# Kernel optimization log

Measured on AMD Instinct MI355X. Metric: run time of the kernel, lower is better.

## Reference

```python
import jax, jax.numpy as jnp
import numpy as np

N, E, DIM, NF, ED = 15000, 30000, 64, 3, 1

def _gru_cell(x, h, w_ih, w_hh, b_ih, b_hh):
    gi = x @ w_ih.T + b_ih
    gh = h @ w_hh.T + b_hh
    ir, iz, i_n = jnp.split(gi, 3, axis=-1)
    hr, hz, hn = jnp.split(gh, 3, axis=-1)
    r = jax.nn.sigmoid(ir + hr)
    z = jax.nn.sigmoid(iz + hz)
    n = jnp.tanh(i_n + r * hn)
    return (1.0 - z) * n + z * h

def _lstm_cell(x, h, c, w_ih, w_hh, b_ih, b_hh):
    g = x @ w_ih.T + b_ih + h @ w_hh.T + b_hh
    i, f, gg, o = jnp.split(g, 4, axis=-1)
    c2 = jax.nn.sigmoid(f) * c + jax.nn.sigmoid(i) * jnp.tanh(gg)
    return jax.nn.sigmoid(o) * jnp.tanh(c2), c2

def setup_inputs():
    key = jax.random.key(0)
    ks = jax.random.split(key, 32)
    p = lambda k, shape: jax.random.normal(k, shape, jnp.float32) * 0.05
    return {
        "x": jax.random.normal(ks[0], (N, NF), jnp.float32),
        "edge_index": jax.random.randint(ks[1], (2, E), 0, N),
        "edge_attr": jax.random.uniform(ks[2], (E, ED), jnp.float32),
        "lin0_w": p(ks[3], (DIM, NF)), "lin0_b": p(ks[4], (DIM,)),
        "e1_w": p(ks[5], (DIM, ED)), "e1_b": p(ks[6], (DIM,)),
        "e2_w": p(ks[7], (DIM * DIM, DIM)), "e2_b": p(ks[8], (DIM * DIM,)),
        "root_w": p(ks[9], (DIM, DIM)), "conv_b": p(ks[10], (DIM,)),
        "gru_w_ih": p(ks[11], (3 * DIM, DIM)), "gru_w_hh": p(ks[12], (3 * DIM, DIM)),
        "gru_b_ih": p(ks[13], (3 * DIM,)), "gru_b_hh": p(ks[14], (3 * DIM,)),
        "s2s_w_ih": p(ks[15], (4 * DIM, 2 * DIM)), "s2s_w_hh": p(ks[16], (4 * DIM, DIM)),
        "s2s_b_ih": p(ks[17], (4 * DIM,)), "s2s_b_hh": p(ks[18], (4 * DIM,)),
        "mem_w_ih": p(ks[19], (4 * DIM, 2 * DIM)), "mem_w_hh": p(ks[20], (4 * DIM, DIM)),
        "mem_b_ih": p(ks[21], (4 * DIM,)), "mem_b_hh": p(ks[22], (4 * DIM,)),
        "lin1_w": p(ks[23], (DIM, DIM)), "lin1_b": p(ks[24], (DIM,)),
        "lin3_w": p(ks[25], (1, DIM)), "lin3_b": p(ks[26], (1,)),
    }

def reference(x, edge_index, edge_attr, lin0_w, lin0_b, e1_w, e1_b, e2_w, e2_b,
              root_w, conv_b, gru_w_ih, gru_w_hh, gru_b_ih, gru_b_hh,
              s2s_w_ih, s2s_w_hh, s2s_b_ih, s2s_b_hh,
              mem_w_ih, mem_w_hh, mem_b_ih, mem_b_hh,
              lin1_w, lin1_b, lin3_w, lin3_b):
    n = x.shape[0]
    src, dst = edge_index[0], edge_index[1]
    # per-edge weight matrices from the edge MLP: [E, DIM, DIM] (edge_attr is constant across the 6 conv steps)
    he = jax.nn.relu(edge_attr @ e1_w.T + e1_b)
    We = (he @ e2_w.T + e2_b).reshape(-1, DIM, DIM)
    deg = jax.ops.segment_sum(jnp.ones(src.shape[0], jnp.float32), dst, num_segments=n)
    denom = jnp.maximum(deg, 1.0)[:, None]
    out = jax.nn.relu(x @ lin0_w.T + lin0_b)   # [N, DIM]
    h = out                                    # GRU hidden init = lin0 output
    for _ in range(6):
        msg = jnp.einsum('ei,eio->eo', out[src], We)          # gather + per-edge matmul
        agg = jax.ops.segment_sum(msg, dst, num_segments=n) / denom  # mean aggr
        m = jax.nn.relu(agg + out @ root_w + conv_b)          # NNConv root + bias
        h = _gru_cell(m, h, gru_w_ih, gru_w_hh, gru_b_ih, gru_b_hh)
        out = h
    # Set2Set pooling over a single graph (data.batch is all zeros)
    q_star = jnp.zeros((1, 2 * DIM), x.dtype)
    hs = jnp.zeros((1, DIM), x.dtype)
    cs = jnp.zeros((1, DIM), x.dtype)
    for _ in range(6):
        hs, cs = _lstm_cell(q_star, hs, cs, s2s_w_ih, s2s_w_hh, s2s_b_ih, s2s_b_hh)
        e = out @ hs[0]                     # [N] attention logits
        a = jax.nn.softmax(e)
        r = (a[:, None] * out).sum(0, keepdims=True)  # [1, DIM]
        q_star = jnp.concatenate([hs, r], axis=-1)     # [1, 2*DIM]
    hx, cx = _lstm_cell(q_star, jnp.zeros((1, DIM), x.dtype), jnp.zeros((1, DIM), x.dtype),
                        mem_w_ih, mem_w_hh, mem_b_ih, mem_b_hh)
    o = jax.nn.relu(hx @ lin1_w.T + lin1_b)
    v = o @ lin3_w.T + lin3_b               # [1, 1]
    return v, hx, cx
```

## Files before the change

### kernel.cpp

```cpp
#include <hip/hip_runtime.h>
#include <math.h>

#define Nn 15000
#define NP 15040
#define Ee 30000
#define NB_E 118
#define EB 938

#define OFF_AGG   0
#define OFF_DEG   962560
#define ZERO_END  977560
#define OFF_OUT   977568
#define OFF_DINV  1940128
#define OFF_AT    1955136
#define OFF_BT    2221376
#define OFF_PE    2496016
#define OFF_BH    2526016
#define OFF_SS    2541376
#define OFF_SD    2571376
#define OFF_SA    2601376
#define OFF_SP    2631376
#define OFF_PK    2661376
#define OFF_GMA   2690048
#define OFF_GSA   2690304
#define OFF_GRA   2690560
#define OFF_GMB   2706944
#define OFF_GSB   2707200
#define OFF_GRB   2707456
#define OFF_TSA   2723968
#define OFF_TSB   2740352
#define OFF_TMA   2756736
#define OFF_TMB   2773120
#define OFF_HSA   2789504
#define OFF_CSA   2789568
#define OFF_HSB   2789632
#define OFF_CSB   2789696
#define WS_FLOATS 2789760

#define SA_L0_END   3760
#define SA_WT2_END  3872
#define SA_WT3_END  4128
#define SA_Z_END    5083
#define SA_AB_END   6123
#define SA_EP_END   6241
#define ZERO_F4     244390

__device__ __forceinline__ float sigf(float x) { return 1.0f / (1.0f + expf(-x)); }
__device__ __forceinline__ float bcast(float v, int l) {
    return __int_as_float(__builtin_amdgcn_readlane(__float_as_int(v), l));
}
__device__ __forceinline__ int bcasti(int v, int l) {
    return __builtin_amdgcn_readlane(v, l);
}

__global__ __launch_bounds__(256) void k_setupAll(
        const float* __restrict__ x, const float* __restrict__ l0w,
        const float* __restrict__ l0b, float* __restrict__ out,
        const float* __restrict__ e1w, const float* __restrict__ e1b,
        const float* __restrict__ e2w, const float* __restrict__ e2b,
        float* __restrict__ At, float* __restrict__ Bt,
        const float* __restrict__ rootw, const float* __restrict__ whh,
        const float* __restrict__ wih, float* __restrict__ pk,
        const float* __restrict__ swih, const float* __restrict__ swhh,
        const float* __restrict__ mwih,
        float* __restrict__ tsa, float* __restrict__ tsb,
        float* __restrict__ tma, float* __restrict__ tmb,
        float* __restrict__ zbase,
        const int* __restrict__ ei, const float* __restrict__ ea,
        float* __restrict__ deg, int* __restrict__ pe, int* __restrict__ bh) {
    int b = blockIdx.x, tid = threadIdx.x;
    if (b < SA_L0_END) {
        int idx = b*256 + tid;
        int n = idx >> 6, o = idx & 63;
        float vv = 0.f;
        if (n < Nn)
            vv = fmaxf(l0b[o] + x[n*3+0]*l0w[o*3+0] + x[n*3+1]*l0w[o*3+1]
                       + x[n*3+2]*l0w[o*3+2], 0.f);
        out[idx] = vv;
    } else if (b < SA_WT2_END) {
        int idx = (b - SA_L0_END)*256 + tid;
        int g = idx >> 12;
        int t2 = idx & 4095;
        int q4 = t2 >> 2, k = t2 & 3;
        int lane = q4 & 63;
        int i4 = q4 >> 6;
        int i = i4*4 + k;
        float vv;
        if (g == 0)      vv = rootw[i*64 + lane];
        else if (g < 4)  vv = whh[((g-1)*64 + lane)*64 + i];
        else             vv = wih[((g-4)*64 + lane)*64 + i];
        pk[idx] = vv;
    } else if (b < SA_WT3_END) {
        int idx = (b - SA_WT2_END)*256 + tid;
        int t2 = idx >> 14, r = idx & 16383;
        int i = r >> 8, g = r & 255;
        if (t2 == 0)      tsa[r] = swih[g*128 + i] + swhh[g*64 + i];
        else if (t2 == 1) tsb[r] = swih[g*128 + 64 + i];
        else if (t2 == 2) tma[r] = mwih[g*128 + i];
        else              tmb[r] = mwih[g*128 + 64 + i];
    } else if (b < SA_Z_END) {
        int idx = (b - SA_WT3_END)*256 + tid;
        if (idx < ZERO_F4)
            ((float4*)zbase)[idx] = make_float4(0.f, 0.f, 0.f, 0.f);
    } else if (b < SA_AB_END) {
        __shared__ float t[64]; __shared__ int valid[64];
        __shared__ float sbp[65]; __shared__ int cnt;
        __shared__ float su[64], sv[64];
        int rel = b - SA_Z_END;
        int j = rel >> 4, qc = rel & 15;
        float w1 = 0.f, b1 = 0.f, tv = 0.f; int va = 0;
        if (tid < 64) {
            w1 = e1w[tid]; b1 = e1b[tid];
            if (w1 != 0.f) { tv = -b1 / w1; va = (tv > 0.f && tv < 1.f) ? 1 : 0; }
            t[tid] = tv; valid[tid] = va;
        }
        __syncthreads();
        if (tid < 64 && va) {
            int rank = 0;
            for (int kk = 0; kk < 64; ++kk)
                if (valid[kk] && (t[kk] < tv || (t[kk] == tv && kk < tid))) rank++;
            sbp[rank] = tv;
        }
        if (tid == 0) { int c = 0; for (int kk = 0; kk < 64; ++kk) c += valid[kk]; cnt = c; }
        __syncthreads();
        int m = cnt;
        if (j > m) return;
        if (tid < 64) {
            float lo = (j == 0) ? 0.f : sbp[j-1];
            float hi = (j == m) ? 1.f : sbp[j];
            float c = 0.5f * (lo + hi);
            int msk = (c * w1 + b1) > 0.f;
            su[tid] = msk ? w1 : 0.f;
            sv[tid] = msk ? b1 : 0.f;
        }
        __syncthreads();
        int q = qc*256 + tid;
        int i = q >> 6, o = q & 63;
        const float* row = e2w + q*64;
        float a = 0.f, bb = 0.f;
        #pragma unroll 8
        for (int k = 0; k < 64; ++k) { float w = row[k]; a = fmaf(su[k], w, a); bb = fmaf(sv[k], w, bb); }
        At[j*4096 + o*64 + i] = a;
        Bt[j*4096 + o*64 + i] = bb + e2b[q];
    } else {
        __shared__ float t[64]; __shared__ int valid[64];
        __shared__ float sbp[65]; __shared__ int cnt;
        __shared__ int lh[65];
        int eb = b - SA_AB_END;
        float w1 = 0.f, b1 = 0.f, tv = 0.f; int va = 0;
        if (tid < 64) {
            w1 = e1w[tid]; b1 = e1b[tid];
            if (w1 != 0.f) { tv = -b1 / w1; va = (tv > 0.f && tv < 1.f) ? 1 : 0; }
            t[tid] = tv; valid[tid] = va;
        }
        if (tid < 65) lh[tid] = 0;
        __syncthreads();
        if (tid < 64 && va) {
            int rank = 0;
            for (int kk = 0; kk < 64; ++kk)
                if (valid[kk] && (t[kk] < tv || (t[kk] == tv && kk < tid))) rank++;
            sbp[rank] = tv;
        }
        if (tid == 0) { int c = 0; for (int kk = 0; kk < 64; ++kk) c += valid[kk]; cnt = c; }
        __syncthreads();
        int m = cnt;
        int e = eb * 256 + tid;
        if (e < Ee) {
            atomicAdd(&deg[ei[Ee + e]], 1.0f);
            float a = ea[e];
            int p = 0;
            for (int jj = 0; jj < m; ++jj) p += (sbp[jj] <= a) ? 1 : 0;
            pe[e] = p;
            atomicAdd(&lh[p], 1);
        }
        __syncthreads();
        if (tid < 65) bh[eb*65 + tid] = lh[tid];
    }
}

__global__ __launch_bounds__(256) void k_scatter3(
        const float* __restrict__ deg, float* __restrict__ dinv,
        const int* __restrict__ ei, const float* __restrict__ ea,
        const int* __restrict__ pe, const int* __restrict__ bh,
        int* __restrict__ sS, int* __restrict__ sD,
        float* __restrict__ sA, int* __restrict__ sP) {
    int tid = threadIdx.x;
    if (blockIdx.x < 59) {
        int n = blockIdx.x * 256 + tid;
        if (n < Nn) dinv[n] = 1.0f / fmaxf(deg[n], 1.0f);
        return;
    }
    int eb = blockIdx.x - 59;
    __shared__ int stot[65], sown[65], sbase[65], cur[65];
    if (tid < 65) {
        int own = 0, tot = 0;
        for (int b2 = 0; b2 < NB_E; ++b2) {
            int v = bh[b2*65 + tid];
            if (b2 < eb) own += v;
            tot += v;
        }
        stot[tid] = tot; sown[tid] = own;
    }
    __syncthreads();
    if (tid == 0) {
        int run = 0;
        for (int j = 0; j < 65; ++j) { sbase[j] = run; run += stot[j]; }
    }
    __syncthreads();
    if (tid < 65) cur[tid] = sbase[tid] + sown[tid];
    __syncthreads();
    int e = eb * 256 + tid;
    if (e >= Ee) return;
    int p = pe[e];
    int pos = atomicAdd(&cur[p], 1);
    sS[pos] = ei[e]; sD[pos] = ei[Ee + e]; sA[pos] = ea[e]; sP[pos] = p;
}

__global__ __launch_bounds__(256) void k_edge6(
        const int* __restrict__ sS, const int* __restrict__ sD,
        const float* __restrict__ sA, const int* __restrict__ sP,
        const float* __restrict__ out, const float* __restrict__ At,
        const float* __restrict__ Bt, const float* __restrict__ dinv,
        float* __restrict__ agg) {
    int tid = threadIdx.x, lane = tid & 63;
    int wid = (blockIdx.x * 256 + tid) >> 6;
    int e0 = wid * 8;
    if (e0 >= Ee) return;

    int eidx = e0 + lane;
    int msrc = 0, mdst = 0, mp = 0; float ma = 0.f, mdv = 0.f;
    if (lane < 8) {
        msrc = sS[eidx]; mdst = sD[eidx]; ma = sA[eidx]; mp = sP[eidx];
        mdv = dinv[mdst];
    }

    float hv[8];
    #pragma unroll
    for (int j = 0; j < 8; ++j) hv[j] = out[bcasti(msrc, j)*64 + lane];

    float Ar[64], Br[64];
    int curp = -1;
    #pragma unroll
    for (int j = 0; j < 8; ++j) {
        int p = bcasti(mp, j);
        if (p != curp) {
            curp = p;
            const float4* Ap4 = (const float4*)(At + p*4096 + lane*64);
            const float4* Bp4 = (const float4*)(Bt + p*4096 + lane*64);
            #pragma unroll
            for (int q = 0; q < 16; ++q) {
                float4 av = Ap4[q], bv = Bp4[q];
                Ar[q*4+0]=av.x; Ar[q*4+1]=av.y; Ar[q*4+2]=av.z; Ar[q*4+3]=av.w;
                Br[q*4+0]=bv.x; Br[q*4+1]=bv.y; Br[q*4+2]=bv.z; Br[q*4+3]=bv.w;
            }
        }
        float a = bcast(ma, j);
        float acc0 = 0.f, acc1 = 0.f, acc2 = 0.f, acc3 = 0.f;
        #pragma unroll
        for (int i = 0; i < 64; i += 4) {
            acc0 = fmaf(bcast(hv[j], i+0), fmaf(a, Ar[i+0], Br[i+0]), acc0);
            acc1 = fmaf(bcast(hv[j], i+1), fmaf(a, Ar[i+1], Br[i+1]), acc1);
            acc2 = fmaf(bcast(hv[j], i+2), fmaf(a, Ar[i+2], Br[i+2]), acc2);
            acc3 = fmaf(bcast(hv[j], i+3), fmaf(a, Ar[i+3], Br[i+3]), acc3);
        }
        float acc = ((acc0 + acc1) + (acc2 + acc3)) * bcast(mdv, j);
        atomicAdd(&agg[bcasti(mdst, j)*64 + lane], acc);
    }
}

__global__ __launch_bounds__(512, 2) void k_gru9(
        float* __restrict__ out, float* __restrict__ agg,
        const float* __restrict__ pk, const float* __restrict__ convb,
        const float* __restrict__ gbih, const float* __restrict__ gbhh) {
    __shared__ __align__(16) float wL[7*4096];
    int tid = threadIdx.x, lane = tid & 63, w = tid >> 6;
    int n0 = blockIdx.x*64 + w*8;

    float hv[8], av[8];
    #pragma unroll
    for (int k = 0; k < 8; ++k) hv[k] = out[(n0+k)*64 + lane];
    #pragma unroll
    for (int k = 0; k < 8; ++k) {
        int gi = (n0+k)*64 + lane;
        av[k] = agg[gi];
        agg[gi] = 0.f;
    }

    {
        const float4* src = (const float4*)pk;
        float4* dst = (float4*)wL;
        #pragma unroll
        for (int i = 0; i < 14; ++i) dst[i*512 + tid] = src[i*512 + tid];
    }
    __syncthreads();
    const float4* wL4 = (const float4*)wL;

    float mv[8], ghr[8], ghz[8], ghn[8];
    float a0[8], a1[8], a2[8], a3[8];
    #pragma unroll
    for (int k = 0; k < 8; ++k) { a0[k]=0.f; a1[k]=0.f; a2[k]=0.f; a3[k]=0.f; }
    #pragma unroll 4
    for (int i4 = 0; i4 < 16; ++i4) {
        float4 w0 = wL4[(0*16+i4)*64 + lane];
        float4 w1 = wL4[(1*16+i4)*64 + lane];
        float4 w2 = wL4[(2*16+i4)*64 + lane];
        float4 w3 = wL4[(3*16+i4)*64 + lane];
        #pragma unroll
        for (int k = 0; k < 8; ++k) {
            float h;
            h = bcast(hv[k], i4*4+0);
            a0[k]=fmaf(h,w0.x,a0[k]); a1[k]=fmaf(h,w1.x,a1[k]);
            a2[k]=fmaf(h,w2.x,a2[k]); a3[k]=fmaf(h,w3.x,a3[k]);
            h = bcast(hv[k], i4*4+1);
            a0[k]=fmaf(h,w0.y,a0[k]); a1[k]=fmaf(h,w1.y,a1[k]);
            a2[k]=fmaf(h,w2.y,a2[k]); a3[k]=fmaf(h,w3.y,a3[k]);
            h = bcast(hv[k], i4*4+2);
            a0[k]=fmaf(h,w0.z,a0[k]); a1[k]=fmaf(h,w1.z,a1[k]);
            a2[k]=fmaf(h,w2.z,a2[k]); a3[k]=fmaf(h,w3.z,a3[k]);
            h = bcast(hv[k], i4*4+3);
            a0[k]=fmaf(h,w0.w,a0[k]); a1[k]=fmaf(h,w1.w,a1[k]);
            a2[k]=fmaf(h,w2.w,a2[k]); a3[k]=fmaf(h,w3.w,a3[k]);
        }
    }
    float cbv = convb[lane];
    #pragma unroll
    for (int k = 0; k < 8; ++k) {
        mv[k] = fmaxf(a0[k] + av[k] + cbv, 0.f);
        ghr[k] = a1[k]; ghz[k] = a2[k]; ghn[k] = a3[k];
    }

    #pragma unroll
    for (int k = 0; k < 8; ++k) { a0[k]=0.f; a1[k]=0.f; a2[k]=0.f; }
    #pragma unroll 4
    for (int i4 = 0; i4 < 16; ++i4) {
        float4 w4v = wL4[(4*16+i4)*64 + lane];
        float4 w5v = wL4[(5*16+i4)*64 + lane];
        float4 w6v = wL4[(6*16+i4)*64 + lane];
        #pragma unroll
        for (int k = 0; k < 8; ++k) {
            float h;
            h = bcast(mv[k], i4*4+0);
            a0[k]=fmaf(h,w4v.x,a0[k]); a1[k]=fmaf(h,w5v.x,a1[k]); a2[k]=fmaf(h,w6v.x,a2[k]);
            h = bcast(mv[k], i4*4+1);
            a0[k]=fmaf(h,w4v.y,a0[k]); a1[k]=fmaf(h,w5v.y,a1[k]); a2[k]=fmaf(h,w6v.y,a2[k]);
            h = bcast(mv[k], i4*4+2);
            a0[k]=fmaf(h,w4v.z,a0[k]); a1[k]=fmaf(h,w5v.z,a1[k]); a2[k]=fmaf(h,w6v.z,a2[k]);
            h = bcast(mv[k], i4*4+3);
            a0[k]=fmaf(h,w4v.w,a0[k]); a1[k]=fmaf(h,w5v.w,a1[k]); a2[k]=fmaf(h,w6v.w,a2[k]);
        }
    }

    float br  = gbih[lane]      + gbhh[lane];
    float bz  = gbih[64+lane]   + gbhh[64+lane];
    float bnI = gbih[128+lane];
    float bnH = gbhh[128+lane];
    #pragma unroll
    for (int k = 0; k < 8; ++k) {
        float r  = sigf(a0[k] + ghr[k] + br);
        float z  = sigf(a1[k] + ghz[k] + bz);
        float nn = tanhf(fmaf(r, ghn[k] + bnH, a2[k] + bnI));
        out[(n0+k)*64 + lane] = (1.f - z)*nn + z*hv[k];
    }
}

__global__ __launch_bounds__(512) void k_s2s(
        const float* __restrict__ tsa, const float* __restrict__ tsb,
        const float* __restrict__ bih, const float* __restrict__ bhh,
        const float* __restrict__ hs_rd, const float* __restrict__ cs_rd,
        float* __restrict__ hs_wr, float* __restrict__ cs_wr,
        const float* __restrict__ out,
        const float* __restrict__ gmax_rd, const float* __restrict__ gsum_rd,
        const float* __restrict__ gr_rd,
        float* __restrict__ gmax_wr, float* __restrict__ gsum_wr,
        float* __restrict__ gr_wr, int it) {
    __shared__ float red[512], shs[64], scs[64], srv[64], sg[256];
    __shared__ float wred[8], zred[8];
    __shared__ float sm_m[8], sm_z[8], sm_r[8][64];
    int tid = threadIdx.x, lane = tid & 63, w = tid >> 6;
    if (it == 0) {
        if (tid < 64) { shs[tid] = 0.f; scs[tid] = 0.f; srv[tid] = 0.f; }
        __syncthreads();
    } else {
        float gm = (tid < 256) ? gmax_rd[tid] : -3.4e38f;
        float wm = gm;
        #pragma unroll
        for (int off = 32; off > 0; off >>= 1) wm = fmaxf(wm, __shfl_xor(wm, off, 64));
        if (lane == 0) wred[w] = wm;
        __syncthreads();
        float M = fmaxf(fmaxf(fmaxf(wred[0], wred[1]), fmaxf(wred[2], wred[3])),
                        fmaxf(fmaxf(wred[4], wred[5]), fmaxf(wred[6], wred[7])));
        float zt = (tid < 256) ? gsum_rd[tid] * expf(gm - M) : 0.f;
        #pragma unroll
        for (int off = 32; off > 0; off >>= 1) zt += __shfl_xor(zt, off, 64);
        if (lane == 0) zred[w] = zt;
        float racc = 0.f;
        for (int b2 = w; b2 < 256; b2 += 8)
            racc = fmaf(gr_rd[b2*64 + lane], expf(gmax_rd[b2] - M), racc);
        red[tid] = racc;
        if (tid < 64) { shs[tid] = hs_rd[tid]; scs[tid] = cs_rd[tid]; }
        __syncthreads();
        if (w == 0) {
            float Z = zred[0]+zred[1]+zred[2]+zred[3]+zred[4]+zred[5]+zred[6]+zred[7];
            float s = 0.f;
            #pragma unroll
            for (int k = 0; k < 8; ++k) s += red[k*64 + lane];
            srv[lane] = s / Z;
        }
        __syncthreads();
    }
    if (tid < 256) {
        float g = bih[tid] + bhh[tid];
        #pragma unroll 8
        for (int i = 0; i < 64; ++i)
            g += shs[i]*tsa[i*256 + tid] + srv[i]*tsb[i*256 + tid];
        sg[tid] = g;
    }
    __syncthreads();
    if (tid < 64) {
        float ii = sigf(sg[tid]), ff = sigf(sg[64+tid]);
        float gg = tanhf(sg[128+tid]), oo = sigf(sg[192+tid]);
        float c2 = ff*scs[tid] + ii*gg;
        float hn = oo*tanhf(c2);
        shs[tid] = hn;
        if (blockIdx.x == 0) { hs_wr[tid] = hn; cs_wr[tid] = c2; }
    }
    __syncthreads();
    float hsv = shs[lane];
    float m = -3.4e38f, Z2 = 0.f, racc2 = 0.f;
    for (int n = blockIdx.x*8 + w; n < Nn; n += 2048) {
        float ov = out[n*64 + lane];
        float p = ov * hsv;
        #pragma unroll
        for (int off = 32; off > 0; off >>= 1) p += __shfl_xor(p, off, 64);
        float mn = fmaxf(m, p);
        float sc = expf(m - mn);
        float t  = expf(p - mn);
        Z2 = fmaf(Z2, sc, t);
        racc2 = fmaf(racc2, sc, t*ov);
        m = mn;
    }
    if (lane == 0) { sm_m[w] = m; sm_z[w] = Z2; }
    sm_r[w][lane] = racc2;
    __syncthreads();
    if (w == 0) {
        float M = sm_m[0];
        #pragma unroll
        for (int j = 1; j < 8; ++j) M = fmaxf(M, sm_m[j]);
        float Zb = 0.f, rb = 0.f;
        #pragma unroll
        for (int j = 0; j < 8; ++j) {
            float e = expf(sm_m[j] - M);
            Zb = fmaf(sm_z[j], e, Zb);
            rb = fmaf(sm_r[j][lane], e, rb);
        }
        gr_wr[blockIdx.x*64 + lane] = rb;
        if (lane == 0) { gmax_wr[blockIdx.x] = M; gsum_wr[blockIdx.x] = Zb; }
    }
}

__global__ __launch_bounds__(256) void k_final2(
        const float* __restrict__ tma, const float* __restrict__ tmb,
        const float* __restrict__ mbih, const float* __restrict__ mbhh,
        const float* __restrict__ hs,
        const float* __restrict__ gmax, const float* __restrict__ gsum,
        const float* __restrict__ gr,
        const float* __restrict__ l1w, const float* __restrict__ l1b,
        const float* __restrict__ l3w, const float* __restrict__ l3b,
        float* __restrict__ dout) {
    __shared__ float red[256], shs[64], srv[64], sg[256], shx[64], so[64];
    __shared__ float wred[4], zred[4];
    int tid = threadIdx.x, lane = tid & 63, w = tid >> 6;
    {
        float gm = gmax[tid];
        float wm = gm;
        #pragma unroll
        for (int off = 32; off > 0; off >>= 1) wm = fmaxf(wm, __shfl_xor(wm, off, 64));
        if (lane == 0) wred[w] = wm;
        __syncthreads();
        float M = fmaxf(fmaxf(wred[0], wred[1]), fmaxf(wred[2], wred[3]));
        float zt = gsum[tid] * expf(gm - M);
        #pragma unroll
        for (int off = 32; off > 0; off >>= 1) zt += __shfl_xor(zt, off, 64);
        if (lane == 0) zred[w] = zt;
        float racc = 0.f;
        for (int b2 = w; b2 < 256; b2 += 4)
            racc = fmaf(gr[b2*64 + lane], expf(gmax[b2] - M), racc);
        red[tid] = racc;
        if (tid < 64) shs[tid] = hs[tid];
        __syncthreads();
        if (w == 0) {
            float Z = zred[0]+zred[1]+zred[2]+zred[3];
            srv[lane] = (red[lane] + red[64+lane] + red[128+lane] + red[192+lane]) / Z;
        }
    }
    __syncthreads();
    {
        float g = mbih[tid] + mbhh[tid];
        #pragma unroll 8
        for (int i = 0; i < 64; ++i)
            g += shs[i]*tma[i*256 + tid] + srv[i]*tmb[i*256 + tid];
        sg[tid] = g;
    }
    __syncthreads();
    if (tid < 64) {
        float ii = sigf(sg[tid]);
        float gg = tanhf(sg[128+tid]);
        float oo = sigf(sg[192+tid]);
        float c2 = ii * gg;
        float hx = oo * tanhf(c2);
        shx[tid] = hx;
        dout[1 + tid] = hx;
        dout[65 + tid] = c2;
    }
    __syncthreads();
    if (tid < 64) {
        float a = l1b[tid];
        const float* wr = l1w + tid*64;
        #pragma unroll 8
        for (int i = 0; i < 64; ++i) a = fmaf(shx[i], wr[i], a);
        so[tid] = fmaxf(a, 0.f);
    }
    __syncthreads();
    if (tid == 0) {
        float v = l3b[0];
        for (int i = 0; i < 64; ++i) v = fmaf(so[i], l3w[i], v);
        dout[0] = v;
    }
}

extern "C" void kernel_launch(void* const* d_in, const int* in_sizes, int n_in,
                              void* d_out, int out_size, void* d_ws, size_t ws_size,
                              hipStream_t stream) {
    const float* x    = (const float*)d_in[0];
    const int*   ei   = (const int*)  d_in[1];
    const float* ea   = (const float*)d_in[2];
    const float* l0w  = (const float*)d_in[3];
    const float* l0b  = (const float*)d_in[4];
    const float* e1w  = (const float*)d_in[5];
    const float* e1b  = (const float*)d_in[6];
    const float* e2w  = (const float*)d_in[7];
    const float* e2b  = (const float*)d_in[8];
    const float* rootw= (const float*)d_in[9];
    const float* convb= (const float*)d_in[10];
    const float* gwih = (const float*)d_in[11];
    const float* gwhh = (const float*)d_in[12];
    const float* gbih = (const float*)d_in[13];
    const float* gbhh = (const float*)d_in[14];
    const float* swih = (const float*)d_in[15];
    const float* swhh = (const float*)d_in[16];
    const float* sbih = (const float*)d_in[17];
    const float* sbhh = (const float*)d_in[18];
    const float* mwih = (const float*)d_in[19];
    const float* mbih = (const float*)d_in[21];
    const float* mbhh = (const float*)d_in[22];
    const float* l1w  = (const float*)d_in[23];
    const float* l1b  = (const float*)d_in[24];
    const float* l3w  = (const float*)d_in[25];
    const float* l3b  = (const float*)d_in[26];

    float* ws   = (float*)d_ws;
    float* dout = (float*)d_out;
    if (ws_size < (size_t)WS_FLOATS * sizeof(float)) return;

    float* agg  = ws + OFF_AGG;
    float* deg  = ws + OFF_DEG;
    float* out  = ws + OFF_OUT;
    float* dinv = ws + OFF_DINV;
    float* At   = ws + OFF_AT;
    float* Bt   = ws + OFF_BT;
    int*   pe   = (int*)(ws + OFF_PE);
    int*   bh   = (int*)(ws + OFF_BH);
    int*   sS   = (int*)(ws + OFF_SS);
    int*   sD   = (int*)(ws + OFF_SD);
    float* sA   = ws + OFF_SA;
    int*   sP   = (int*)(ws + OFF_SP);
    float* pk   = ws + OFF_PK;
    float* gmA  = ws + OFF_GMA;
    float* gsA  = ws + OFF_GSA;
    float* grA  = ws + OFF_GRA;
    float* gmB  = ws + OFF_GMB;
    float* gsB  = ws + OFF_GSB;
    float* grB  = ws + OFF_GRB;
    float* tsa  = ws + OFF_TSA;
    float* tsb  = ws + OFF_TSB;
    float* tma  = ws + OFF_TMA;
    float* tmb  = ws + OFF_TMB;
    float* hsA  = ws + OFF_HSA;
    float* csA  = ws + OFF_CSA;
    float* hsB  = ws + OFF_HSB;
    float* csB  = ws + OFF_CSB;

    k_setupAll<<<SA_EP_END, 256, 0, stream>>>(x, l0w, l0b, out, e1w, e1b, e2w, e2b,
                                              At, Bt, rootw, gwhh, gwih, pk,
                                              swih, swhh, mwih, tsa, tsb, tma, tmb,
                                              ws + OFF_AGG, ei, ea, deg, pe, bh);
    k_scatter3<<<59 + NB_E, 256, 0, stream>>>(deg, dinv, ei, ea, pe, bh,
                                              sS, sD, sA, sP);

    for (int s = 0; s < 6; ++s) {
        k_edge6<<<EB, 256, 0, stream>>>(sS, sD, sA, sP, out, At, Bt, dinv, agg);
        k_gru9 <<<NP/64, 512, 0, stream>>>(out, agg, pk, convb, gbih, gbhh);
    }

    for (int it = 0; it < 6; ++it) {
        float* gm_rd = (it & 1) ? gmA : gmB;
        float* gs_rd = (it & 1) ? gsA : gsB;
        float* gr_rd = (it & 1) ? grA : grB;
        float* hs_rd = (it & 1) ? hsA : hsB;
        float* cs_rd = (it & 1) ? csA : csB;
        float* gm_wr = (it & 1) ? gmB : gmA;
        float* gs_wr = (it & 1) ? gsB : gsA;
        float* gr_wr = (it & 1) ? grB : grA;
        float* hs_wr = (it & 1) ? hsB : hsA;
        float* cs_wr = (it & 1) ? csB : csA;
        k_s2s<<<256, 512, 0, stream>>>(tsa, tsb, sbih, sbhh, hs_rd, cs_rd,
                                       hs_wr, cs_wr, out,
                                       gm_rd, gs_rd, gr_rd, gm_wr, gs_wr, gr_wr, it);
    }

    k_final2<<<1, 256, 0, stream>>>(tma, tmb, mbih, mbhh, hsB, gmB, gsB, grB,
                                    l1w, l1b, l3w, l3b, dout);
}
```

Measured before the change: 431.6 us.

## Stage per-pattern edge weight matrices in shared memory for block-wide reuse

Result: faster. 420.1 us, median of 2 (-2.7%).

```diff
diff --git a/kernel.cpp b/kernel.cpp
--- a/kernel.cpp
+++ b/kernel.cpp
@@ -5,7 +5,7 @@
 #define NP 15040
 #define Ee 30000
 #define NB_E 118
-#define EB 938
+#define EB7 938
 
 #define OFF_AGG   0
 #define OFF_DEG   962560
@@ -140,8 +140,9 @@
         float a = 0.f, bb = 0.f;
         #pragma unroll 8
         for (int k = 0; k < 64; ++k) { float w = row[k]; a = fmaf(su[k], w, a); bb = fmaf(sv[k], w, bb); }
-        At[j*4096 + o*64 + i] = a;
-        Bt[j*4096 + o*64 + i] = bb + e2b[q];
+        int oidx = j*4096 + (i >> 2)*256 + o*4 + (i & 3);
+        At[oidx] = a;
+        Bt[oidx] = bb + e2b[q];
     } else {
         __shared__ float t[64]; __shared__ int valid[64];
         __shared__ float sbp[65]; __shared__ int cnt;
@@ -216,55 +217,77 @@
     sS[pos] = ei[e]; sD[pos] = ei[Ee + e]; sA[pos] = ea[e]; sP[pos] = p;
 }
 
-__global__ __launch_bounds__(256) void k_edge6(
+__global__ __launch_bounds__(256) void k_edge7(
         const int* __restrict__ sS, const int* __restrict__ sD,
         const float* __restrict__ sA, const int* __restrict__ sP,
         const float* __restrict__ out, const float* __restrict__ At,
         const float* __restrict__ Bt, const float* __restrict__ dinv,
         float* __restrict__ agg) {
-    int tid = threadIdx.x, lane = tid & 63;
-    int wid = (blockIdx.x * 256 + tid) >> 6;
-    int e0 = wid * 8;
-    if (e0 >= Ee) return;
-
-    int eidx = e0 + lane;
-    int msrc = 0, mdst = 0, mp = 0; float ma = 0.f, mdv = 0.f;
-    if (lane < 8) {
-        msrc = sS[eidx]; mdst = sD[eidx]; ma = sA[eidx]; mp = sP[eidx];
-        mdv = dinv[mdst];
-    }
-
-    float hv[8];
+    __shared__ __align__(16) float sW[8192];
+    __shared__ int spat[32];
+    int tid = threadIdx.x, lane = tid & 63, w = tid >> 6;
+    int e0b = blockIdx.x * 32;
+    int nE = Ee - e0b; if (nE > 32) nE = 32;
+    if (tid < 32) spat[tid] = (tid < nE) ? sP[e0b + tid] : -1;
+
+    int je = w * 8;
+    int msrc = 0, mdst = 0; float ma = 0.f, mdv = 0.f;
+    if (lane < 8 && je + lane < nE) {
+        int eidx = e0b + je + lane;
+        msrc = sS[eidx]; mdst = sD[eidx]; ma = sA[eidx]; mdv = dinv[mdst];
+    }
+    float hv[8], av[8], dv[8];
     #pragma unroll
     for (int j = 0; j < 8; ++j) hv[j] = out[bcasti(msrc, j)*64 + lane];
-
-    float Ar[64], Br[64];
-    int curp = -1;
-    #pragma unroll
-    for (int j = 0; j < 8; ++j) {
-        int p = bcasti(mp, j);
-        if (p != curp) {
-            curp = p;
-            const float4* Ap4 = (const float4*)(At + p*4096 + lane*64);
-            const float4* Bp4 = (const float4*)(Bt + p*4096 + lane*64);
+    #pragma unroll
+    for (int j = 0; j < 8; ++j) { av[j] = bcast(ma, j); dv[j] = bcast(mdv, j); }
+    __syncthreads();
+
+    int ss = 0;
+    while (ss < nE) {
+        int p = spat[ss];
+        int se = ss + 1;
+        while (se < nE && spat[se] == p) ++se;
+        __syncthreads();
+        {
+            const float4* srcA = (const float4*)(At + p*4096);
+            const float4* srcB = (const float4*)(Bt + p*4096);
+            float4* dA = (float4*)sW;
+            float4* dB = (float4*)(sW + 4096);
             #pragma unroll
-            for (int q = 0; q < 16; ++q) {
-                float4 av = Ap4[q], bv = Bp4[q];
-                Ar[q*4+0]=av.x; Ar[q*4+1]=av.y; Ar[q*4+2]=av.z; Ar[q*4+3]=av.w;
-                Br[q*4+0]=bv.x; Br[q*4+1]=bv.y; Br[q*4+2]=bv.z; Br[q*4+3]=bv.w;
+            for (int i = 0; i < 4; ++i) {
+                dA[i*256 + tid] = srcA[i*256 + tid];
+                dB[i*256 + tid] = srcB[i*256 + tid];
             }
         }
-        float a = bcast(ma, j);
-        float acc0 = 0.f, acc1 = 0.f, acc2 = 0.f, acc3 = 0.f;
-        #pragma unroll
-        for (int i = 0; i < 64; i += 4) {
-            acc0 = fmaf(bcast(hv[j], i+0), fmaf(a, Ar[i+0], Br[i+0]), acc0);
-            acc1 = fmaf(bcast(hv[j], i+1), fmaf(a, Ar[i+1], Br[i+1]), acc1);
-            acc2 = fmaf(bcast(hv[j], i+2), fmaf(a, Ar[i+2], Br[i+2]), acc2);
-            acc3 = fmaf(bcast(hv[j], i+3), fmaf(a, Ar[i+3], Br[i+3]), acc3);
-        }
-        float acc = ((acc0 + acc1) + (acc2 + acc3)) * bcast(mdv, j);
-        atomicAdd(&agg[bcasti(mdst, j)*64 + lane], acc);
+        __syncthreads();
+
+        float acc[8];
+        #pragma unroll
+        for (int j = 0; j < 8; ++j) acc[j] = 0.f;
+        const float4* A4p = (const float4*)sW;
+        const float4* B4p = (const float4*)(sW + 4096);
+        #pragma unroll 4
+        for (int i4 = 0; i4 < 16; ++i4) {
+            float4 a4 = A4p[i4*64 + lane];
+            float4 b4 = B4p[i4*64 + lane];
+            #pragma unroll
+            for (int j = 0; j < 8; ++j) {
+                float aj = av[j];
+                float h;
+                h = bcast(hv[j], i4*4+0); acc[j] = fmaf(h, fmaf(aj, a4.x, b4.x), acc[j]);
+                h = bcast(hv[j], i4*4+1); acc[j] = fmaf(h, fmaf(aj, a4.y, b4.y), acc[j]);
+                h = bcast(hv[j], i4*4+2); acc[j] = fmaf(h, fmaf(aj, a4.z, b4.z), acc[j]);
+                h = bcast(hv[j], i4*4+3); acc[j] = fmaf(h, fmaf(aj, a4.w, b4.w), acc[j]);
+            }
+        }
+        #pragma unroll
+        for (int j = 0; j < 8; ++j) {
+            int jj = je + j;
+            if (jj >= ss && jj < se)
+                atomicAdd(&agg[bcasti(mdst, j)*64 + lane], acc[j] * dv[j]);
+        }
+        ss = se;
     }
 }
 
@@ -598,7 +621,7 @@
                                               sS, sD, sA, sP);
 
     for (int s = 0; s < 6; ++s) {
-        k_edge6<<<EB, 256, 0, stream>>>(sS, sD, sA, sP, out, At, Bt, dinv, agg);
+        k_edge7<<<EB7, 256, 0, stream>>>(sS, sD, sA, sP, out, At, Bt, dinv, agg);
         k_gru9 <<<NP/64, 512, 0, stream>>>(out, agg, pk, convb, gbih, gbhh);
     }
 
```
